# Performance work log

Hardware: AMD Instinct MI355X
Metric: run time of the kernel (lower is better)

The kernel has to match this reference:

```python
import jax, jax.numpy as jnp
import numpy as np

B, S, H, DK, DV, D = 1024, 8, 16, 32, 32, 512


def setup_inputs() -> dict:
    key = jax.random.key(0)
    ks = jax.random.split(key, 12)
    s = 1.0 / np.sqrt(D)
    return {
        "Q": jax.random.normal(ks[0], (B, S, D), jnp.float32),
        "K": jax.random.normal(ks[1], (B, S, D), jnp.float32),
        "V": jax.random.normal(ks[2], (B, S, D), jnp.float32),
        "attn_mask": jax.random.bernoulli(ks[3], 0.2, (B, S, S)),
        "hyper": jax.random.normal(ks[4], (B, H * S * DK), jnp.float32),
        "Wq": jax.random.normal(ks[5], (H * DK, D), jnp.float32) * s,
        "bq": jnp.zeros((H * DK,), jnp.float32),
        "Wk": jax.random.normal(ks[6], (H * DK, D), jnp.float32) * s,
        "bk": jnp.zeros((H * DK,), jnp.float32),
        "Wv": jax.random.normal(ks[7], (H * DV, D), jnp.float32) * s,
        "bv": jnp.zeros((H * DV,), jnp.float32),
        "Wo": jax.random.normal(ks[8], (D, H * DV), jnp.float32) * s,
        "bo": jnp.zeros((D,), jnp.float32),
        "ln_g": jnp.ones((D,), jnp.float32),
        "ln_b": jnp.zeros((D,), jnp.float32),
    }


def reference(Q, K, V, attn_mask, hyper, Wq, bq, Wk, bk, Wv, bv, Wo, bo, ln_g, ln_b):
    # QKV projections -> [B, H, S, dk]
    q = (Q @ Wq.T + bq).reshape(B, S, H, DK).transpose(0, 2, 1, 3)
    k = (K @ Wk.T + bk).reshape(B, S, H, DK).transpose(0, 2, 1, 3)
    v = (V @ Wv.T + bv).reshape(B, S, H, DV).transpose(0, 2, 1, 3)
    # scaled dot-product attention with mask
    scores = jnp.einsum('bhqd,bhkd->bhqk', q, k) / np.sqrt(DK).astype(np.float32)
    scores = jnp.where(attn_mask[:, None, :, :], -1e9, scores)
    weights = jax.nn.softmax(scores, axis=-1)
    # hyper-gated AV
    context = jnp.einsum('bhqk,bhkd->bhqd', weights, v) * hyper.reshape(B, H, S, DK)
    context = context.transpose(0, 2, 1, 3).reshape(B, S, H * DV)
    # output projection + residual layernorm (eps=1e-5)
    out = context @ Wo.T + bo + Q
    mu = out.mean(axis=-1, keepdims=True)
    var = out.var(axis=-1, keepdims=True)
    out = (out - mu) * jax.lax.rsqrt(var + 1e-5) * ln_g + ln_b
    return (out, weights)
```

## Files before the change

### kernel.cpp

```cpp
#include <hip/hip_runtime.h>
#include <hip/hip_bf16.h>
#include <cstdint>

#define NB 1024
#define ND 512
#define NM 8192

typedef __attribute__((ext_vector_type(8))) short short8;
typedef __attribute__((ext_vector_type(8))) __bf16 bf16x8;
typedef __attribute__((ext_vector_type(4))) float f32x4;
typedef __attribute__((ext_vector_type(4))) unsigned short ushort4v;

__device__ __forceinline__ unsigned short f2bf(float f) {
  uint32_t x = __builtin_bit_cast(uint32_t, f);
  x += 0x7fffu + ((x >> 16) & 1u);
  return (unsigned short)(x >> 16);
}
__device__ __forceinline__ float bf2f(unsigned short u) {
  return __builtin_bit_cast(float, (uint32_t)u << 16);
}
__device__ __forceinline__ f32x4 mfma16(short8 a, short8 b, f32x4 c) {
  return __builtin_amdgcn_mfma_f32_16x16x32_bf16(
      __builtin_bit_cast(bf16x8, a), __builtin_bit_cast(bf16x8, b), c, 0, 0, 0);
}
__device__ __forceinline__ short8 cvt8(float4 a, float4 b) {
  short8 r;
  r[0] = (short)f2bf(a.x); r[1] = (short)f2bf(a.y);
  r[2] = (short)f2bf(a.z); r[3] = (short)f2bf(a.w);
  r[4] = (short)f2bf(b.x); r[5] = (short)f2bf(b.y);
  r[6] = (short)f2bf(b.z); r[7] = (short)f2bf(b.w);
  return r;
}
__device__ __forceinline__ void gl_lds16(const unsigned short* g, unsigned short* lds) {
  __builtin_amdgcn_global_load_lds(
      (const __attribute__((address_space(1))) unsigned int*)g,
      (__attribute__((address_space(3))) unsigned int*)lds, 16, 0, 0);
}
#define VMCNT(n) asm volatile("s_waitcnt vmcnt(" #n ")" ::: "memory")
#define LGKM0() asm volatile("s_waitcnt lgkmcnt(0)" ::: "memory")
#define BAR() __builtin_amdgcn_s_barrier()

__global__ __launch_bounds__(256) void convert_w(
    const float* __restrict__ Wq, const float* __restrict__ Wk,
    const float* __restrict__ Wv, const float* __restrict__ Wo,
    unsigned short* __restrict__ Wqb, unsigned short* __restrict__ Wkb,
    unsigned short* __restrict__ Wvb, unsigned short* __restrict__ Wob) {
  const int idx = blockIdx.x * 256 + threadIdx.x;
  const int sel = idx >> 15, o = (idx & 32767) * 8;
  const float* src = sel == 0 ? Wq : sel == 1 ? Wk : sel == 2 ? Wv : Wo;
  unsigned short* dst = sel == 0 ? Wqb : sel == 1 ? Wkb : sel == 2 ? Wvb : Wob;
  const float4 a = ((const float4*)(src + o))[0];
  const float4 b = ((const float4*)(src + o))[1];
  *(short8*)(dst + o) = cvt8(a, b);
}

__global__ __launch_bounds__(512, 4) void gemm_qkv(
    const float* __restrict__ Qf, const float* __restrict__ Kf,
    const float* __restrict__ Vf,
    const unsigned short* __restrict__ Wqb, const unsigned short* __restrict__ Wkb,
    const unsigned short* __restrict__ Wvb,
    const float* __restrict__ bq, const float* __restrict__ bk,
    const float* __restrict__ bv,
    unsigned short* __restrict__ qo, unsigned short* __restrict__ ko,
    unsigned short* __restrict__ vo) {
  __shared__ unsigned short Als0[128 * 32], Als1[128 * 32];
  __shared__ unsigned short Wls0[256 * 32], Wls1[256 * 32];

  const int bid = blockIdx.x;
  const int lid = (bid & 7) * 48 + (bid >> 3);
  const int mt = lid / 6, np = lid % 6;
  const int seg = np >> 1, nloc = np & 1;
  const float* A = seg == 0 ? Qf : seg == 1 ? Kf : Vf;
  const unsigned short* W = seg == 0 ? Wqb : seg == 1 ? Wkb : Wvb;
  const float* bias = seg == 0 ? bq : seg == 1 ? bk : bv;
  unsigned short* C = seg == 0 ? qo : seg == 1 ? ko : vo;
  const int mBase = mt * 128, nBase = nloc * 256;

  const int tid = threadIdx.x, lane = tid & 63, wid = tid >> 6;
  const int wm = wid >> 2, wn = wid & 3;
  const int l15 = lane & 15, l4 = lane >> 4;

  const int ar = tid >> 2, ag = tid & 3;
  const float* Aptr = A + (size_t)(mBase + ar) * ND + ag * 8;
  const unsigned short* Wsrc0 =
      W + (size_t)(nBase + wid * 32 + (lane >> 2)) * ND + (lane & 3) * 8;
  const unsigned short* Wsrc1 = Wsrc0 + (size_t)16 * ND;

  f32x4 acc[4][4] = {};
  float4 pa0, pa1;

#define ISSA(kt)                                    \
  {                                                 \
    pa0 = *(const float4*)(Aptr + (kt) * 32);       \
    pa1 = *(const float4*)(Aptr + (kt) * 32 + 4);   \
  }
#define WRA(ALS) { *(short8*)&ALS[ar * 32 + ag * 8] = cvt8(pa0, pa1); }
#define GLW(kt, WLS)                                          \
  {                                                           \
    gl_lds16(Wsrc0 + (kt) * 32, WLS + wid * 1024);            \
    gl_lds16(Wsrc1 + (kt) * 32, WLS + wid * 1024 + 512);      \
  }

  auto compute = [&](const unsigned short* AL, const unsigned short* WL) {
    short8 af[4], bf4[4];
#pragma unroll
    for (int mf = 0; mf < 4; ++mf)
      af[mf] = *(const short8*)&AL[(wm * 64 + mf * 16 + l15) * 32 + l4 * 8];
#pragma unroll
    for (int nf = 0; nf < 4; ++nf)
      bf4[nf] = *(const short8*)&WL[(wn * 64 + nf * 16 + l15) * 32 + l4 * 8];
#pragma unroll
    for (int mf = 0; mf < 4; ++mf)
#pragma unroll
      for (int nf = 0; nf < 4; ++nf)
        acc[mf][nf] = mfma16(af[mf], bf4[nf], acc[mf][nf]);
  };

  ISSA(0); GLW(0, Wls0);
  VMCNT(2);
  WRA(Als0);
  ISSA(1); GLW(1, Wls1);
  VMCNT(4);
  LGKM0(); BAR();

#pragma unroll
  for (int t = 0; t < 16; ++t) {
    compute(t & 1 ? Als1 : Als0, t & 1 ? Wls1 : Wls0);
    if (t < 15) {
      VMCNT(2);
      if (t & 1) { WRA(Als0); } else { WRA(Als1); }
      if (t + 2 < 16) { ISSA(t + 2); VMCNT(2); } else { VMCNT(0); }
      LGKM0(); BAR();
      if (t + 2 < 16) {
        if (t & 1) { GLW(t + 2, Wls1); } else { GLW(t + 2, Wls0); }
      }
    }
  }

#pragma unroll
  for (int nf = 0; nf < 4; ++nf) {
    const int gn = nBase + wn * 64 + nf * 16 + l15;
    const float bb = bias[gn];
#pragma unroll
    for (int mf = 0; mf < 4; ++mf)
#pragma unroll
      for (int r = 0; r < 4; ++r) {
        const int gm = mBase + wm * 64 + mf * 16 + l4 * 4 + r;
        C[(size_t)gm * ND + gn] = f2bf(acc[mf][nf][r] + bb);
      }
  }
#undef ISSA
#undef WRA
#undef GLW
}

__global__ __launch_bounds__(512, 4) void gemm_wo(
    const unsigned short* __restrict__ ctx, const unsigned short* __restrict__ Wob,
    const float* __restrict__ bo, const float* __restrict__ Qres,
    float* __restrict__ out) {
  __shared__ unsigned short Als0[128 * 32], Als1[128 * 32];
  __shared__ unsigned short Wls0[128 * 32], Wls1[128 * 32];

  const int bid = blockIdx.x;
  const int lid = (bid & 7) * 32 + (bid >> 3);
  const int mt = lid >> 2, nloc = lid & 3;
  const int mBase = mt * 128, nBase = nloc * 128;

  const int tid = threadIdx.x, lane = tid & 63, wid = tid >> 6;
  const int wm = wid >> 2, wn = wid & 3;
  const int l15 = lane & 15, l4 = lane >> 4;

  const unsigned short* Asrc =
      ctx + (size_t)(mBase + wid * 16 + (lane >> 2)) * ND + (lane & 3) * 8;
  const unsigned short* Wsrc =
      Wob + (size_t)(nBase + wid * 16 + (lane >> 2)) * ND + (lane & 3) * 8;

  f32x4 acc[4][2] = {};

#define GLAW(kt, ALS, WLS)                          \
  {                                                 \
    gl_lds16(Asrc + (kt) * 32, ALS + wid * 512);    \
    gl_lds16(Wsrc + (kt) * 32, WLS + wid * 512);    \
  }

  auto compute = [&](const unsigned short* AL, const unsigned short* WL) {
    short8 af[4], bf4[2];
#pragma unroll
    for (int mf = 0; mf < 4; ++mf)
      af[mf] = *(const short8*)&AL[(wm * 64 + mf * 16 + l15) * 32 + l4 * 8];
#pragma unroll
    for (int nf = 0; nf < 2; ++nf)
      bf4[nf] = *(const short8*)&WL[(wn * 32 + nf * 16 + l15) * 32 + l4 * 8];
#pragma unroll
    for (int mf = 0; mf < 4; ++mf)
#pragma unroll
      for (int nf = 0; nf < 2; ++nf)
        acc[mf][nf] = mfma16(af[mf], bf4[nf], acc[mf][nf]);
  };

  GLAW(0, Als0, Wls0);
  GLAW(1, Als1, Wls1);
  VMCNT(2);
  BAR();

#pragma unroll
  for (int t = 0; t < 16; ++t) {
    compute(t & 1 ? Als1 : Als0, t & 1 ? Wls1 : Wls0);
    if (t < 15) {
      VMCNT(0);
      BAR();
      if (t + 2 < 16) {
        if (t & 1) { GLAW(t + 2, Als1, Wls1); } else { GLAW(t + 2, Als0, Wls0); }
      }
    }
  }

#pragma unroll
  for (int nf = 0; nf < 2; ++nf) {
    const int gn = nBase + wn * 32 + nf * 16 + l15;
    const float bb = bo[gn];
#pragma unroll
    for (int mf = 0; mf < 4; ++mf)
#pragma unroll
      for (int r = 0; r < 4; ++r) {
        const int gm = mBase + wm * 64 + mf * 16 + l4 * 4 + r;
        out[(size_t)gm * ND + gn] =
            acc[mf][nf][r] + bb + Qres[(size_t)gm * ND + gn];
      }
  }
#undef GLAW
}

__global__ __launch_bounds__(256) void attn_kernel(
    const unsigned short* __restrict__ q, const unsigned short* __restrict__ k,
    const unsigned short* __restrict__ v, const int* __restrict__ mask,
    const float* __restrict__ hyper, float* __restrict__ wout,
    unsigned short* __restrict__ ctx) {
  const int tid = threadIdx.x;
  const int wid = tid >> 6, lane = tid & 63;
  const int t = blockIdx.x * 4 + wid;
  const int b = t >> 4, h = t & 15;
  const int i = lane >> 3, j = lane & 7;

  const unsigned short* qrow = q + (size_t)(b * 8 + i) * ND + h * 32;
  const unsigned short* krow = k + (size_t)(b * 8 + j) * ND + h * 32;
  float dot = 0.f;
#pragma unroll
  for (int c = 0; c < 4; ++c) {
    const short8 qv = ((const short8*)qrow)[c];
    const short8 kv = ((const short8*)krow)[c];
#pragma unroll
    for (int e = 0; e < 8; ++e)
      dot += bf2f((unsigned short)qv[e]) * bf2f((unsigned short)kv[e]);
  }
  float score = dot * 0.17677669529663687f;
  if (mask[b * 64 + i * 8 + j]) score = -1e9f;

  float mx = score;
#pragma unroll
  for (int o = 4; o; o >>= 1) mx = fmaxf(mx, __shfl_xor(mx, o, 8));
  const float e = __expf(score - mx);
  float sm = e;
#pragma unroll
  for (int o = 4; o; o >>= 1) sm += __shfl_xor(sm, o, 8);
  const float w = e / sm;
  wout[(size_t)t * 64 + lane] = w;

  const int d0 = (lane & 7) * 4;
  float c0 = 0, c1 = 0, c2 = 0, c3 = 0;
#pragma unroll
  for (int jj = 0; jj < 8; ++jj) {
    const float wj = __shfl(w, jj, 8);
    const ushort4v vv = *(const ushort4v*)(v + (size_t)(b * 8 + jj) * ND + h * 32 + d0);
    c0 += wj * bf2f(vv[0]); c1 += wj * bf2f(vv[1]);
    c2 += wj * bf2f(vv[2]); c3 += wj * bf2f(vv[3]);
  }
  const float4 hv = *(const float4*)(hyper + (size_t)b * 4096 + h * 256 + i * 32 + d0);
  ushort4v co;
  co[0] = f2bf(c0 * hv.x); co[1] = f2bf(c1 * hv.y);
  co[2] = f2bf(c2 * hv.z); co[3] = f2bf(c3 * hv.w);
  *(ushort4v*)(ctx + (size_t)(b * 8 + i) * ND + h * 32 + d0) = co;
}

__global__ __launch_bounds__(256) void ln_kernel(float* __restrict__ io,
                                                 const float* __restrict__ g,
                                                 const float* __restrict__ be) {
  const int tid = threadIdx.x, wid = tid >> 6, lane = tid & 63;
  const size_t row = (size_t)blockIdx.x * 4 + wid;
  float* prow = io + row * ND + lane * 8;
  float4 x0 = ((float4*)prow)[0], x1 = ((float4*)prow)[1];
  float s = x0.x + x0.y + x0.z + x0.w + x1.x + x1.y + x1.z + x1.w;
  float sq = x0.x * x0.x + x0.y * x0.y + x0.z * x0.z + x0.w * x0.w +
             x1.x * x1.x + x1.y * x1.y + x1.z * x1.z + x1.w * x1.w;
#pragma unroll
  for (int o = 32; o; o >>= 1) {
    s += __shfl_xor(s, o, 64);
    sq += __shfl_xor(sq, o, 64);
  }
  const float mu = s * (1.f / 512.f);
  const float inv = rsqrtf(sq * (1.f / 512.f) - mu * mu + 1e-5f);
  const float4 g0 = ((const float4*)(g + lane * 8))[0];
  const float4 g1 = ((const float4*)(g + lane * 8))[1];
  const float4 e0 = ((const float4*)(be + lane * 8))[0];
  const float4 e1 = ((const float4*)(be + lane * 8))[1];
  float4 o0, o1;
  o0.x = (x0.x - mu) * inv * g0.x + e0.x; o0.y = (x0.y - mu) * inv * g0.y + e0.y;
  o0.z = (x0.z - mu) * inv * g0.z + e0.z; o0.w = (x0.w - mu) * inv * g0.w + e0.w;
  o1.x = (x1.x - mu) * inv * g1.x + e1.x; o1.y = (x1.y - mu) * inv * g1.y + e1.y;
  o1.z = (x1.z - mu) * inv * g1.z + e1.z; o1.w = (x1.w - mu) * inv * g1.w + e1.w;
  ((float4*)prow)[0] = o0;
  ((float4*)prow)[1] = o1;
}

extern "C" void kernel_launch(void* const* d_in, const int* in_sizes, int n_in,
                              void* d_out, int out_size, void* d_ws, size_t ws_size,
                              hipStream_t stream) {
  const float* Q = (const float*)d_in[0];
  const float* K = (const float*)d_in[1];
  const float* V = (const float*)d_in[2];
  const int* msk = (const int*)d_in[3];
  const float* hyper = (const float*)d_in[4];
  const float* Wq = (const float*)d_in[5];
  const float* bq = (const float*)d_in[6];
  const float* Wk = (const float*)d_in[7];
  const float* bk = (const float*)d_in[8];
  const float* Wv = (const float*)d_in[9];
  const float* bv = (const float*)d_in[10];
  const float* Wo = (const float*)d_in[11];
  const float* bo = (const float*)d_in[12];
  const float* lg = (const float*)d_in[13];
  const float* lb = (const float*)d_in[14];

  float* out = (float*)d_out;
  float* wout = out + (size_t)NM * ND;

  const size_t MAT = (size_t)NM * ND;
  unsigned short* qb = (unsigned short*)d_ws;
  unsigned short* kb = qb + MAT;
  unsigned short* vb = kb + MAT;
  unsigned short* ctxb = vb + MAT;
  unsigned short* Wqb = ctxb + MAT;
  unsigned short* Wkb = Wqb + (size_t)ND * ND;
  unsigned short* Wvb = Wkb + (size_t)ND * ND;
  unsigned short* Wob = Wvb + (size_t)ND * ND;

  convert_w<<<512, 256, 0, stream>>>(Wq, Wk, Wv, Wo, Wqb, Wkb, Wvb, Wob);
  gemm_qkv<<<384, 512, 0, stream>>>(Q, K, V, Wqb, Wkb, Wvb,
                                    bq, bk, bv, qb, kb, vb);
  attn_kernel<<<4096, 256, 0, stream>>>(qb, kb, vb, msk, hyper, wout, ctxb);
  gemm_wo<<<256, 512, 0, stream>>>(ctxb, Wob, bo, Q, out);
  ln_kernel<<<2048, 256, 0, stream>>>(out, lg, lb);
}
```

Before: 69.43 us.

## Triple-buffer LDS tiles in QKV and output-projection GEMMs

Both GEMM kernels move from double to triple buffering of the A and W tiles in shared memory. Loads run three k-steps ahead, with vmcnt waits retuned so more global traffic stays in flight behind the MFMA work. The larger LDS footprint lowers the occupancy hints in launch_bounds (from 4 to 2 blocks per CU for gemm_qkv and 3 for gemm_wo), trading occupancy for latency hiding.

```diff
diff --git a/kernel.cpp b/kernel.cpp
--- a/kernel.cpp
+++ b/kernel.cpp
@@ -54,7 +54,7 @@
   *(short8*)(dst + o) = cvt8(a, b);
 }
 
-__global__ __launch_bounds__(512, 4) void gemm_qkv(
+__global__ __launch_bounds__(512, 2) void gemm_qkv(
     const float* __restrict__ Qf, const float* __restrict__ Kf,
     const float* __restrict__ Vf,
     const unsigned short* __restrict__ Wqb, const unsigned short* __restrict__ Wkb,
@@ -63,8 +63,8 @@
     const float* __restrict__ bv,
     unsigned short* __restrict__ qo, unsigned short* __restrict__ ko,
     unsigned short* __restrict__ vo) {
-  __shared__ unsigned short Als0[128 * 32], Als1[128 * 32];
-  __shared__ unsigned short Wls0[256 * 32], Wls1[256 * 32];
+  __shared__ unsigned short Asb[3][128 * 32];
+  __shared__ unsigned short Wsb[3][256 * 32];
 
   const int bid = blockIdx.x;
   const int lid = (bid & 7) * 48 + (bid >> 3);
@@ -87,18 +87,22 @@
   const unsigned short* Wsrc1 = Wsrc0 + (size_t)16 * ND;
 
   f32x4 acc[4][4] = {};
-  float4 pa0, pa1;
-
-#define ISSA(kt)                                    \
-  {                                                 \
-    pa0 = *(const float4*)(Aptr + (kt) * 32);       \
-    pa1 = *(const float4*)(Aptr + (kt) * 32 + 4);   \
-  }
-#define WRA(ALS) { *(short8*)&ALS[ar * 32 + ag * 8] = cvt8(pa0, pa1); }
-#define GLW(kt, WLS)                                          \
-  {                                                           \
-    gl_lds16(Wsrc0 + (kt) * 32, WLS + wid * 1024);            \
-    gl_lds16(Wsrc1 + (kt) * 32, WLS + wid * 1024 + 512);      \
+  float4 pa[3][2];
+
+#define ISSA(kt)                                                  \
+  {                                                               \
+    pa[(kt) % 3][0] = *(const float4*)(Aptr + (kt) * 32);         \
+    pa[(kt) % 3][1] = *(const float4*)(Aptr + (kt) * 32 + 4);     \
+  }
+#define WRA(kt)                                                   \
+  {                                                               \
+    *(short8*)&Asb[(kt) % 3][ar * 32 + ag * 8] =                  \
+        cvt8(pa[(kt) % 3][0], pa[(kt) % 3][1]);                   \
+  }
+#define GLW(kt)                                                   \
+  {                                                               \
+    gl_lds16(Wsrc0 + (kt) * 32, &Wsb[(kt) % 3][wid * 1024]);      \
+    gl_lds16(Wsrc1 + (kt) * 32, &Wsb[(kt) % 3][wid * 1024 + 512]);\
   }
 
   auto compute = [&](const unsigned short* AL, const unsigned short* WL) {
@@ -116,24 +120,30 @@
         acc[mf][nf] = mfma16(af[mf], bf4[nf], acc[mf][nf]);
   };
 
-  ISSA(0); GLW(0, Wls0);
-  VMCNT(2);
-  WRA(Als0);
-  ISSA(1); GLW(1, Wls1);
-  VMCNT(4);
+  ISSA(0); GLW(0);
+  ISSA(1); GLW(1);
+  ISSA(2); GLW(2);
+  VMCNT(10);
+  WRA(0);
+  VMCNT(8);
   LGKM0(); BAR();
 
 #pragma unroll
   for (int t = 0; t < 16; ++t) {
-    compute(t & 1 ? Als1 : Als0, t & 1 ? Wls1 : Wls0);
+    compute(Asb[t % 3], Wsb[t % 3]);
     if (t < 15) {
-      VMCNT(2);
-      if (t & 1) { WRA(Als0); } else { WRA(Als1); }
-      if (t + 2 < 16) { ISSA(t + 2); VMCNT(2); } else { VMCNT(0); }
+      if (t <= 13) { VMCNT(6); } else { VMCNT(2); }
+      WRA(t + 1);
+      if (t <= 12) {
+        ISSA(t + 3);
+        VMCNT(6);
+      } else if (t == 13) {
+        VMCNT(4);
+      } else {
+        VMCNT(0);
+      }
       LGKM0(); BAR();
-      if (t + 2 < 16) {
-        if (t & 1) { GLW(t + 2, Wls1); } else { GLW(t + 2, Wls0); }
-      }
+      if (t <= 12) GLW(t + 3);
     }
   }
 
@@ -154,12 +164,12 @@
 #undef GLW
 }
 
-__global__ __launch_bounds__(512, 4) void gemm_wo(
+__global__ __launch_bounds__(512, 3) void gemm_wo(
     const unsigned short* __restrict__ ctx, const unsigned short* __restrict__ Wob,
     const float* __restrict__ bo, const float* __restrict__ Qres,
     float* __restrict__ out) {
-  __shared__ unsigned short Als0[128 * 32], Als1[128 * 32];
-  __shared__ unsigned short Wls0[128 * 32], Wls1[128 * 32];
+  __shared__ unsigned short Asb[3][128 * 32];
+  __shared__ unsigned short Wsb[3][128 * 32];
 
   const int bid = blockIdx.x;
   const int lid = (bid & 7) * 32 + (bid >> 3);
@@ -177,10 +187,10 @@
 
   f32x4 acc[4][2] = {};
 
-#define GLAW(kt, ALS, WLS)                          \
-  {                                                 \
-    gl_lds16(Asrc + (kt) * 32, ALS + wid * 512);    \
-    gl_lds16(Wsrc + (kt) * 32, WLS + wid * 512);    \
+#define GLAW(kt)                                              \
+  {                                                           \
+    gl_lds16(Asrc + (kt) * 32, &Asb[(kt) % 3][wid * 512]);    \
+    gl_lds16(Wsrc + (kt) * 32, &Wsb[(kt) % 3][wid * 512]);    \
   }
 
   auto compute = [&](const unsigned short* AL, const unsigned short* WL) {
@@ -198,20 +208,17 @@
         acc[mf][nf] = mfma16(af[mf], bf4[nf], acc[mf][nf]);
   };
 
-  GLAW(0, Als0, Wls0);
-  GLAW(1, Als1, Wls1);
-  VMCNT(2);
+  GLAW(0); GLAW(1); GLAW(2);
+  VMCNT(4);
   BAR();
 
 #pragma unroll
   for (int t = 0; t < 16; ++t) {
-    compute(t & 1 ? Als1 : Als0, t & 1 ? Wls1 : Wls0);
+    compute(Asb[t % 3], Wsb[t % 3]);
     if (t < 15) {
-      VMCNT(0);
+      if (t <= 13) { VMCNT(2); } else { VMCNT(0); }
       BAR();
-      if (t + 2 < 16) {
-        if (t & 1) { GLAW(t + 2, Als1, Wls1); } else { GLAW(t + 2, Als0, Wls0); }
-      }
+      if (t <= 12) GLAW(t + 3);
     }
   }
 
```

Result: no change. 68.93 us (median of 2 runs) (-0.7%).
